# Performance work log

Measured on AMD Instinct MI355X. Metric: run time of the kernel, lower is better.

The kernel has to match this reference:

```python
import jax, jax.numpy as jnp
import numpy as np

N_NODES = 100000
N_EDGES = 1000000
IN_DIM, HID_DIM, OUT_DIM = 64, 64, 128


def gcn_conv(x, W, b, src, dst, deg_inv_sqrt, n_nodes):
    # PyG GCNConv: x' = D^{-1/2} (A + I) D^{-1/2} (x W) + b
    xw = x @ W  # [N, out]
    norm = deg_inv_sqrt[src] * deg_inv_sqrt[dst]  # [E'] (edges incl. self-loops)
    msgs = xw[src] * norm[:, None]  # gather + scale, [E', out]
    out = jax.ops.segment_sum(msgs, dst, num_segments=n_nodes)
    return out + b


def setup_inputs() -> dict:
    key = jax.random.key(0)
    ks = jax.random.split(key, 8)
    x = jax.random.normal(ks[0], (N_NODES, IN_DIM), dtype=jnp.float32)
    edge_index = jax.random.randint(ks[1], (2, N_EDGES), 0, N_NODES, dtype=jnp.int64 if jax.config.read('jax_enable_x64') else jnp.int32)
    # Glorot-ish init for weights, zeros for biases (matches GCNConv defaults)
    def glorot(k, fan_in, fan_out):
        s = jnp.sqrt(6.0 / (fan_in + fan_out))
        return jax.random.uniform(k, (fan_in, fan_out), jnp.float32, -s, s)
    return {
        "x": x,
        "W1": glorot(ks[2], IN_DIM, HID_DIM), "b1": jnp.zeros((HID_DIM,), jnp.float32),
        "W2": glorot(ks[3], HID_DIM, HID_DIM), "b2": jnp.zeros((HID_DIM,), jnp.float32),
        "W3": glorot(ks[4], HID_DIM, OUT_DIM), "b3": jnp.zeros((OUT_DIM,), jnp.float32),
        "edge_index": edge_index,
    }


def reference(x, W1, b1, W2, b2, W3, b3, edge_index):
    n = x.shape[0]
    loop = jnp.arange(n, dtype=edge_index.dtype)
    src = jnp.concatenate([edge_index[0], loop])  # add self-loops
    dst = jnp.concatenate([edge_index[1], loop])
    deg = jax.ops.segment_sum(jnp.ones_like(dst, dtype=x.dtype), dst, num_segments=n)
    deg_inv_sqrt = jnp.where(deg > 0, jax.lax.rsqrt(deg), 0.0)
    # Dropout(p=0.5) is identity in eval mode
    h = jax.nn.relu(gcn_conv(x, W1, b1, src, dst, deg_inv_sqrt, n))
    h = jax.nn.relu(gcn_conv(h, W2, b2, src, dst, deg_inv_sqrt, n))
    return gcn_conv(h, W3, b3, src, dst, deg_inv_sqrt, n)
```

## Files before the change

### kernel.cpp

```cpp
#include <hip/hip_runtime.h>
#include <hip/hip_fp16.h>


#define NBMAX 512
#define EPB   4096


__global__ __launch_bounds__(256) void bin_hist(const int* __restrict__ dst,
                                                int* __restrict__ hist, int E, int NB) {
  __shared__ int cnt[NBMAX];
  for (int i = threadIdx.x; i < NB; i += 256) cnt[i] = 0;
  __syncthreads();
  int base = blockIdx.x * EPB;
  for (int it = 0; it < EPB; it += 256) {
    int e = base + it + threadIdx.x;
    if (e < E) atomicAdd(&cnt[dst[e] >> 8], 1);
  }
  __syncthreads();
  for (int i = threadIdx.x; i < NB; i += 256) hist[(size_t)blockIdx.x * NB + i] = cnt[i];
}

__global__ __launch_bounds__(256) void bucket_prefix(int* __restrict__ hist,
                                                     int* __restrict__ bucket_tot,
                                                     int nblk, int NB) {
  __shared__ int tmp[256];
  int b = blockIdx.x;
  int t = threadIdx.x;
  int v = (t < nblk) ? hist[(size_t)t * NB + b] : 0;
  tmp[t] = v;
  __syncthreads();
  for (int off = 1; off < 256; off <<= 1) {
    int a = (t >= off) ? tmp[t - off] : 0;
    __syncthreads();
    tmp[t] += a;
    __syncthreads();
  }
  if (t < nblk) hist[(size_t)t * NB + b] = tmp[t] - v;
  if (t == 255) bucket_tot[b] = tmp[255];
}

__global__ __launch_bounds__(512) void bucket_scan(const int* __restrict__ bucket_tot,
                                                   int* __restrict__ bucket_off, int NB, int E) {
  __shared__ int tmp[NBMAX];
  int t = threadIdx.x;
  int v = (t < NB) ? bucket_tot[t] : 0;
  tmp[t] = v;
  __syncthreads();
  for (int off = 1; off < 512; off <<= 1) {
    int a = (t >= off) ? tmp[t - off] : 0;
    __syncthreads();
    tmp[t] += a;
    __syncthreads();
  }
  if (t < NB) bucket_off[t] = tmp[t] - v;
  if (t == 0) bucket_off[NB] = E;
}

__global__ __launch_bounds__(256) void bin_scatter(const int* __restrict__ src,
                                                   const int* __restrict__ dst,
                                                   const int* __restrict__ chunk_excl,
                                                   const int* __restrict__ bucket_off,
                                                   int* __restrict__ pairs, int E, int NB) {
  __shared__ int cur[NBMAX];
  for (int i = threadIdx.x; i < NB; i += 256)
    cur[i] = bucket_off[i] + chunk_excl[(size_t)blockIdx.x * NB + i];
  __syncthreads();
  int base = blockIdx.x * EPB;
  for (int it = 0; it < EPB; it += 256) {
    int e = base + it + threadIdx.x;
    if (e < E) {
      int d = dst[e];
      int pos = atomicAdd(&cur[d >> 8], 1);
      pairs[pos] = src[e] | ((d & 255) << 17);
    }
  }
}

__device__ __forceinline__ unsigned int packh(float a, float b) {
  unsigned int lo = (unsigned int)__half_as_ushort(__float2half_rn(a));
  unsigned int hi = (unsigned int)__half_as_ushort(__float2half_rn(b));
  return lo | (hi << 16);
}

__device__ __forceinline__ void unpack_add(float& x0, float& x1, unsigned int u) {
  x0 += __half2float(__ushort_as_half((unsigned short)(u & 0xffffu)));
  x1 += __half2float(__ushort_as_half((unsigned short)(u >> 16)));
}

__global__ __launch_bounds__(256) void bucket_fill(const int* __restrict__ pairs,
                                                   const int* __restrict__ bucket_off,
                                                   int* __restrict__ row_ptr,
                                                   int* __restrict__ csr_src,
                                                   float* __restrict__ dis,
                                                   const float* __restrict__ x,
                                                   unsigned short* __restrict__ xs,
                                                   int n, int NB) {
  __shared__ int cnt[256];
  __shared__ int tmp[256];
  __shared__ int cur[256];
  __shared__ float sdis[256];
  int b = blockIdx.x;
  int t = threadIdx.x;
  int node_base = b << 8;
  int ebeg = bucket_off[b];
  int eend = bucket_off[b + 1];
  cnt[t] = 0;
  __syncthreads();
  for (int e = ebeg + t; e < eend; e += 256) {
    atomicAdd(&cnt[(pairs[e] >> 17) & 255], 1);
  }
  __syncthreads();
  int v = cnt[t];
  tmp[t] = v;
  __syncthreads();
  for (int off = 1; off < 256; off <<= 1) {
    int a = (t >= off) ? tmp[t - off] : 0;
    __syncthreads();
    tmp[t] += a;
    __syncthreads();
  }
  int excl = tmp[t] - v;
  int node = node_base + t;
  float s = rsqrtf((float)v + 1.0f);
  sdis[t] = s;
  if (node < n) {
    row_ptr[node] = ebeg + excl;
    dis[node] = s;
  }
  cur[t] = ebeg + excl;
  if (b == NB - 1 && t == 0) row_ptr[n] = eend;
  __syncthreads();
  for (int e = ebeg + t; e < eend; e += 256) {
    int p = pairs[e];
    int pos = atomicAdd(&cur[(p >> 17) & 255], 1);
    csr_src[pos] = p & 0x1FFFF;
  }
  int rows = n - node_base;
  if (rows > 256) rows = 256;
  for (int i = t; i < rows * 8; i += 256) {
    int r = i >> 3;
    float sc = sdis[r];
    const float4* p = (const float4*)(x + ((size_t)(node_base + r) * 64) + (i & 7) * 8);
    float4 f0 = p[0];
    float4 f1 = p[1];
    uint4 u;
    u.x = packh(f0.x * sc, f0.y * sc);
    u.y = packh(f0.z * sc, f0.w * sc);
    u.z = packh(f1.x * sc, f1.y * sc);
    u.w = packh(f1.z * sc, f1.w * sc);
    *(uint4*)(xs + (size_t)(node_base + r) * 64 + (i & 7) * 8) = u;
  }
}


__global__ __launch_bounds__(256) void gather64q(const int* __restrict__ row_ptr,
                                                 const int* __restrict__ csr_src,
                                                 const unsigned short* __restrict__ in,
                                                 const float* __restrict__ dis,
                                                 float* __restrict__ agg, int n) {
  int node = blockIdx.x * 16 + (threadIdx.x >> 4);
  int l15 = threadIdx.x & 15;
  int gbase = threadIdx.x & 48;
  if (node >= n) return;

  int beg = row_ptr[node];
  int end = row_ptr[node + 1];

  float a0 = 0.f, a1 = 0.f, a2 = 0.f, a3 = 0.f;

  {
    uint2 q = *(const uint2*)(in + (size_t)node * 64 + l15 * 4);
    unpack_add(a0, a1, q.x); unpack_add(a2, a3, q.y);
  }

  int k = beg;
  for (; k + 16 <= end; k += 16) {
    int idx = csr_src[k + l15];
#pragma unroll
    for (int rr = 0; rr < 16; rr += 2) {
      int s0 = __shfl(idx, gbase + rr);
      int s1 = __shfl(idx, gbase + rr + 1);
      uint2 q0 = *(const uint2*)(in + (size_t)s0 * 64 + l15 * 4);
      uint2 q1 = *(const uint2*)(in + (size_t)s1 * 64 + l15 * 4);
      unpack_add(a0, a1, q0.x); unpack_add(a2, a3, q0.y);
      unpack_add(a0, a1, q1.x); unpack_add(a2, a3, q1.y);
    }
  }
  int cnt = end - k;
  if (cnt > 0) {
    int ii = k + l15;
    int last = end - 1;
    ii = (ii < end) ? ii : last;
    int idx = csr_src[ii];
#pragma unroll
    for (int rr = 0; rr < 16; rr += 2) {
      int s0 = __shfl(idx, gbase + rr);
      int s1 = __shfl(idx, gbase + rr + 1);
      uint2 q0 = *(const uint2*)(in + (size_t)s0 * 64 + l15 * 4);
      uint2 q1 = *(const uint2*)(in + (size_t)s1 * 64 + l15 * 4);
      q0.x = (rr < cnt) ? q0.x : 0u;
      q0.y = (rr < cnt) ? q0.y : 0u;
      q1.x = (rr + 1 < cnt) ? q1.x : 0u;
      q1.y = (rr + 1 < cnt) ? q1.y : 0u;
      unpack_add(a0, a1, q0.x); unpack_add(a2, a3, q0.y);
      unpack_add(a0, a1, q1.x); unpack_add(a2, a3, q1.y);
    }
  }

  float sc = dis[node];
  *(float4*)&agg[(size_t)node * 64 + l15 * 4] =
      make_float4(a0 * sc, a1 * sc, a2 * sc, a3 * sc);
}


__device__ __forceinline__ void fma4(float4& a, float s, const float4 w) {
  a.x = fmaf(s, w.x, a.x);
  a.y = fmaf(s, w.y, a.y);
  a.z = fmaf(s, w.z, a.z);
  a.w = fmaf(s, w.w, a.w);
}

template <bool RELU, bool SCALE, bool OUTH>
__global__ __launch_bounds__(256, 4) void gemm64(const float* __restrict__ X,
                                                 const float* __restrict__ W,
                                                 const float* __restrict__ B,
                                                 const float* __restrict__ dis,
                                                 float* __restrict__ yF,
                                                 unsigned short* __restrict__ yH,
                                                 int n, int ldw) {
  __shared__ float Ws[64 * 64];
  int tid = threadIdx.x;
  int rb = blockIdx.x * 64;
  int cb = blockIdx.y * 64;

  for (int i = tid; i < 1024; i += 256) {
    int k = i >> 4, cq = (i & 15) << 2;
    *(float4*)&Ws[k * 64 + cq] = *(const float4*)&W[(size_t)k * ldw + cb + cq];
  }
  __syncthreads();

  int r0 = (tid >> 4) << 2;
  int c0 = (tid & 15) << 2;
  int gr0 = rb + r0;

  const float* xp0 = X + (size_t)min(gr0 + 0, n - 1) * 64;
  const float* xp1 = X + (size_t)min(gr0 + 1, n - 1) * 64;
  const float* xp2 = X + (size_t)min(gr0 + 2, n - 1) * 64;
  const float* xp3 = X + (size_t)min(gr0 + 3, n - 1) * 64;

  float4 a0 = make_float4(0.f, 0.f, 0.f, 0.f);
  float4 a1 = a0, a2 = a0, a3 = a0;

#pragma unroll 2
  for (int kc = 0; kc < 64; kc += 4) {
    float4 x0 = *(const float4*)(xp0 + kc);
    float4 x1 = *(const float4*)(xp1 + kc);
    float4 x2 = *(const float4*)(xp2 + kc);
    float4 x3 = *(const float4*)(xp3 + kc);
    float4 w0 = *(const float4*)&Ws[(kc + 0) * 64 + c0];
    float4 w1 = *(const float4*)&Ws[(kc + 1) * 64 + c0];
    float4 w2 = *(const float4*)&Ws[(kc + 2) * 64 + c0];
    float4 w3 = *(const float4*)&Ws[(kc + 3) * 64 + c0];
    fma4(a0, x0.x, w0); fma4(a0, x0.y, w1); fma4(a0, x0.z, w2); fma4(a0, x0.w, w3);
    fma4(a1, x1.x, w0); fma4(a1, x1.y, w1); fma4(a1, x1.z, w2); fma4(a1, x1.w, w3);
    fma4(a2, x2.x, w0); fma4(a2, x2.y, w1); fma4(a2, x2.z, w2); fma4(a2, x2.w, w3);
    fma4(a3, x3.x, w0); fma4(a3, x3.y, w1); fma4(a3, x3.z, w2); fma4(a3, x3.w, w3);
  }

  float4 bb = *(const float4*)&B[cb + c0];
#pragma unroll
  for (int ri = 0; ri < 4; ++ri) {
    int gr = gr0 + ri;
    if (gr >= n) break;
    float4 v = (ri == 0) ? a0 : (ri == 1) ? a1 : (ri == 2) ? a2 : a3;
    v.x += bb.x; v.y += bb.y; v.z += bb.z; v.w += bb.w;
    if (RELU) {
      v.x = fmaxf(v.x, 0.f); v.y = fmaxf(v.y, 0.f);
      v.z = fmaxf(v.z, 0.f); v.w = fmaxf(v.w, 0.f);
    }
    if (SCALE) {
      float s = dis[gr];
      v.x *= s; v.y *= s; v.z *= s; v.w *= s;
    }
    if (OUTH) {
      uint2 u;
      u.x = packh(v.x, v.y);
      u.y = packh(v.z, v.w);
      *(uint2*)(yH + (size_t)gr * ldw + cb + c0) = u;
    } else {
      *(float4*)&yF[(size_t)gr * ldw + cb + c0] = v;
    }
  }
}


extern "C" void kernel_launch(void* const* d_in, const int* in_sizes, int n_in,
                              void* d_out, int out_size, void* d_ws, size_t ws_size,
                              hipStream_t stream) {
  const float* x  = (const float*)d_in[0];
  const float* W1 = (const float*)d_in[1];
  const float* b1 = (const float*)d_in[2];
  const float* W2 = (const float*)d_in[3];
  const float* b2 = (const float*)d_in[4];
  const float* W3 = (const float*)d_in[5];
  const float* b3 = (const float*)d_in[6];
  const int*   ei = (const int*)d_in[7];

  const int n = in_sizes[0] / 64;
  const int E = in_sizes[7] / 2;
  const int* src = ei;
  const int* dst = ei + E;

  const int NB    = (n + 255) >> 8;
  const int nblkA = (E + EPB - 1) / EPB;

  float* dis = (float*)d_ws;
  unsigned short* bufIn = (unsigned short*)(dis + n);
  float* agg = (float*)(bufIn + (size_t)n * 64);
  int* row_ptr = (int*)(agg + (size_t)n * 64);
  int* csr_src = row_ptr + (n + 2);
  int* pairs   = csr_src + E;
  int* hist       = pairs + E;
  int* bucket_tot = hist + (size_t)nblkA * NB;
  int* bucket_off = bucket_tot + NB;
  float* out = (float*)d_out;

  dim3 blk(256);
  int gW = (n + 15) / 16;
  int gT = (n + 63) / 64;

  bin_hist<<<nblkA, blk, 0, stream>>>(dst, hist, E, NB);
  bucket_prefix<<<NB, blk, 0, stream>>>(hist, bucket_tot, nblkA, NB);
  bucket_scan<<<1, 512, 0, stream>>>(bucket_tot, bucket_off, NB, E);
  bin_scatter<<<nblkA, blk, 0, stream>>>(src, dst, hist, bucket_off, pairs, E, NB);
  bucket_fill<<<NB, blk, 0, stream>>>(pairs, bucket_off, row_ptr, csr_src, dis, x, bufIn, n, NB);

  gather64q<<<gW, blk, 0, stream>>>(row_ptr, csr_src, bufIn, dis, agg, n);
  gemm64<true, true, true><<<dim3(gT, 1), blk, 0, stream>>>(agg, W1, b1, dis, nullptr, bufIn, n, 64);

  gather64q<<<gW, blk, 0, stream>>>(row_ptr, csr_src, bufIn, dis, agg, n);
  gemm64<true, true, true><<<dim3(gT, 1), blk, 0, stream>>>(agg, W2, b2, dis, nullptr, bufIn, n, 64);

  gather64q<<<gW, blk, 0, stream>>>(row_ptr, csr_src, bufIn, dis, agg, n);
  gemm64<false, false, false><<<dim3(gT, 2), blk, 0, stream>>>(agg, W3, b3, dis, out, nullptr, n, 128);
}
```

Measured before the change: 278.3 us.

## Fuse neighbor gather and dense transform into one per-layer kernel

Merges the aggregation kernel and the following GEMM into a single kernel per layer. Each block aggregates 64 nodes into shared memory, then multiplies that tile by W held in shared memory. This removes the fp32 intermediate aggregate buffer round-trip and three kernel launches. Because a layer now reads and writes the same half-precision feature array, ping-pong buffers are used. The cost is heavier shared memory use (up to about 50KB for the last layer) and a larger gather per block, which may lower occupancy and latency hiding for the random gathers.

```diff
diff --git a/kernel.cpp b/kernel.cpp
--- a/kernel.cpp
+++ b/kernel.cpp
@@ -153,89 +153,73 @@
 }
 
 
-__global__ __launch_bounds__(256) void gather64q(const int* __restrict__ row_ptr,
-                                                 const int* __restrict__ csr_src,
-                                                 const unsigned short* __restrict__ in,
-                                                 const float* __restrict__ dis,
-                                                 float* __restrict__ agg, int n) {
-  int node = blockIdx.x * 16 + (threadIdx.x >> 4);
-  int l15 = threadIdx.x & 15;
-  int gbase = threadIdx.x & 48;
-  if (node >= n) return;
-
-  int beg = row_ptr[node];
-  int end = row_ptr[node + 1];
-
-  float a0 = 0.f, a1 = 0.f, a2 = 0.f, a3 = 0.f;
-
-  {
-    uint2 q = *(const uint2*)(in + (size_t)node * 64 + l15 * 4);
-    unpack_add(a0, a1, q.x); unpack_add(a2, a3, q.y);
-  }
-
-  int k = beg;
-  for (; k + 16 <= end; k += 16) {
-    int idx = csr_src[k + l15];
-#pragma unroll
-    for (int rr = 0; rr < 16; rr += 2) {
-      int s0 = __shfl(idx, gbase + rr);
-      int s1 = __shfl(idx, gbase + rr + 1);
-      uint2 q0 = *(const uint2*)(in + (size_t)s0 * 64 + l15 * 4);
-      uint2 q1 = *(const uint2*)(in + (size_t)s1 * 64 + l15 * 4);
-      unpack_add(a0, a1, q0.x); unpack_add(a2, a3, q0.y);
-      unpack_add(a0, a1, q1.x); unpack_add(a2, a3, q1.y);
-    }
-  }
-  int cnt = end - k;
-  if (cnt > 0) {
-    int ii = k + l15;
-    int last = end - 1;
-    ii = (ii < end) ? ii : last;
-    int idx = csr_src[ii];
-#pragma unroll
-    for (int rr = 0; rr < 16; rr += 2) {
-      int s0 = __shfl(idx, gbase + rr);
-      int s1 = __shfl(idx, gbase + rr + 1);
-      uint2 q0 = *(const uint2*)(in + (size_t)s0 * 64 + l15 * 4);
-      uint2 q1 = *(const uint2*)(in + (size_t)s1 * 64 + l15 * 4);
-      q0.x = (rr < cnt) ? q0.x : 0u;
-      q0.y = (rr < cnt) ? q0.y : 0u;
-      q1.x = (rr + 1 < cnt) ? q1.x : 0u;
-      q1.y = (rr + 1 < cnt) ? q1.y : 0u;
-      unpack_add(a0, a1, q0.x); unpack_add(a2, a3, q0.y);
-      unpack_add(a0, a1, q1.x); unpack_add(a2, a3, q1.y);
-    }
-  }
-
-  float sc = dis[node];
-  *(float4*)&agg[(size_t)node * 64 + l15 * 4] =
-      make_float4(a0 * sc, a1 * sc, a2 * sc, a3 * sc);
-}
-
-
-__device__ __forceinline__ void fma4(float4& a, float s, const float4 w) {
-  a.x = fmaf(s, w.x, a.x);
-  a.y = fmaf(s, w.y, a.y);
-  a.z = fmaf(s, w.z, a.z);
-  a.w = fmaf(s, w.w, a.w);
-}
-
-template <bool RELU, bool SCALE, bool OUTH>
-__global__ __launch_bounds__(256, 4) void gemm64(const float* __restrict__ X,
-                                                 const float* __restrict__ W,
-                                                 const float* __restrict__ B,
-                                                 const float* __restrict__ dis,
-                                                 float* __restrict__ yF,
-                                                 unsigned short* __restrict__ yH,
-                                                 int n, int ldw) {
-  __shared__ float Ws[64 * 64];
+template <bool RELU, bool SCALE, bool OUTH, int NCB>
+__global__ __launch_bounds__(256, 4) void gcn_layer(
+    const int* __restrict__ row_ptr, const int* __restrict__ csr_src,
+    const unsigned short* __restrict__ in, const float* __restrict__ dis,
+    const float* __restrict__ W, const float* __restrict__ Bv,
+    float* __restrict__ yF, unsigned short* __restrict__ yH, int n) {
+  __shared__ float Xs[64 * 68];
+  __shared__ float Ws[64 * 64 * NCB];
   int tid = threadIdx.x;
   int rb = blockIdx.x * 64;
-  int cb = blockIdx.y * 64;
-
-  for (int i = tid; i < 1024; i += 256) {
-    int k = i >> 4, cq = (i & 15) << 2;
-    *(float4*)&Ws[k * 64 + cq] = *(const float4*)&W[(size_t)k * ldw + cb + cq];
+
+  for (int i = tid; i < 64 * 16 * NCB; i += 256) {
+    int k = i / (16 * NCB);
+    int cq = (i % (16 * NCB)) << 2;
+    *(float4*)&Ws[k * (64 * NCB) + cq] = *(const float4*)&W[(size_t)k * (64 * NCB) + cq];
+  }
+
+  int l15 = tid & 15;
+  int gbase = tid & 48;
+  int grp = tid >> 4;
+  for (int it = 0; it < 4; ++it) {
+    int r = it * 16 + grp;
+    int cl = min(rb + r, n - 1);
+    int beg = row_ptr[cl];
+    int end = row_ptr[cl + 1];
+
+    float a0 = 0.f, a1 = 0.f, a2 = 0.f, a3 = 0.f;
+    {
+      uint2 q = *(const uint2*)(in + (size_t)cl * 64 + l15 * 4);
+      unpack_add(a0, a1, q.x); unpack_add(a2, a3, q.y);
+    }
+    int k = beg;
+    for (; k + 16 <= end; k += 16) {
+      int idx = csr_src[k + l15];
+#pragma unroll
+      for (int rr = 0; rr < 16; rr += 2) {
+        int s0 = __shfl(idx, gbase + rr);
+        int s1 = __shfl(idx, gbase + rr + 1);
+        uint2 q0 = *(const uint2*)(in + (size_t)s0 * 64 + l15 * 4);
+        uint2 q1 = *(const uint2*)(in + (size_t)s1 * 64 + l15 * 4);
+        unpack_add(a0, a1, q0.x); unpack_add(a2, a3, q0.y);
+        unpack_add(a0, a1, q1.x); unpack_add(a2, a3, q1.y);
+      }
+    }
+    int cnt = end - k;
+    if (cnt > 0) {
+      int ii = k + l15;
+      int last = end - 1;
+      ii = (ii < end) ? ii : last;
+      int idx = csr_src[ii];
+#pragma unroll
+      for (int rr = 0; rr < 16; rr += 2) {
+        int s0 = __shfl(idx, gbase + rr);
+        int s1 = __shfl(idx, gbase + rr + 1);
+        uint2 q0 = *(const uint2*)(in + (size_t)s0 * 64 + l15 * 4);
+        uint2 q1 = *(const uint2*)(in + (size_t)s1 * 64 + l15 * 4);
+        q0.x = (rr < cnt) ? q0.x : 0u;
+        q0.y = (rr < cnt) ? q0.y : 0u;
+        q1.x = (rr + 1 < cnt) ? q1.x : 0u;
+        q1.y = (rr + 1 < cnt) ? q1.y : 0u;
+        unpack_add(a0, a1, q0.x); unpack_add(a2, a3, q0.y);
+        unpack_add(a0, a1, q1.x); unpack_add(a2, a3, q1.y);
+      }
+    }
+    float sc = dis[cl];
+    *(float4*)&Xs[r * 68 + l15 * 4] =
+        make_float4(a0 * sc, a1 * sc, a2 * sc, a3 * sc);
   }
   __syncthreads();
 
@@ -243,52 +227,79 @@
   int c0 = (tid & 15) << 2;
   int gr0 = rb + r0;
 
-  const float* xp0 = X + (size_t)min(gr0 + 0, n - 1) * 64;
-  const float* xp1 = X + (size_t)min(gr0 + 1, n - 1) * 64;
-  const float* xp2 = X + (size_t)min(gr0 + 2, n - 1) * 64;
-  const float* xp3 = X + (size_t)min(gr0 + 3, n - 1) * 64;
-
-  float4 a0 = make_float4(0.f, 0.f, 0.f, 0.f);
-  float4 a1 = a0, a2 = a0, a3 = a0;
+#pragma unroll
+  for (int cb = 0; cb < NCB; ++cb) {
+    float4 a0 = make_float4(0.f, 0.f, 0.f, 0.f);
+    float4 a1 = a0, a2 = a0, a3 = a0;
 
 #pragma unroll 2
-  for (int kc = 0; kc < 64; kc += 4) {
-    float4 x0 = *(const float4*)(xp0 + kc);
-    float4 x1 = *(const float4*)(xp1 + kc);
-    float4 x2 = *(const float4*)(xp2 + kc);
-    float4 x3 = *(const float4*)(xp3 + kc);
-    float4 w0 = *(const float4*)&Ws[(kc + 0) * 64 + c0];
-    float4 w1 = *(const float4*)&Ws[(kc + 1) * 64 + c0];
-    float4 w2 = *(const float4*)&Ws[(kc + 2) * 64 + c0];
-    float4 w3 = *(const float4*)&Ws[(kc + 3) * 64 + c0];
-    fma4(a0, x0.x, w0); fma4(a0, x0.y, w1); fma4(a0, x0.z, w2); fma4(a0, x0.w, w3);
-    fma4(a1, x1.x, w0); fma4(a1, x1.y, w1); fma4(a1, x1.z, w2); fma4(a1, x1.w, w3);
-    fma4(a2, x2.x, w0); fma4(a2, x2.y, w1); fma4(a2, x2.z, w2); fma4(a2, x2.w, w3);
-    fma4(a3, x3.x, w0); fma4(a3, x3.y, w1); fma4(a3, x3.z, w2); fma4(a3, x3.w, w3);
-  }
-
-  float4 bb = *(const float4*)&B[cb + c0];
+    for (int kc = 0; kc < 64; kc += 4) {
+      float4 x0 = *(const float4*)&Xs[(r0 + 0) * 68 + kc];
+      float4 x1 = *(const float4*)&Xs[(r0 + 1) * 68 + kc];
+      float4 x2 = *(const float4*)&Xs[(r0 + 2) * 68 + kc];
+      float4 x3 = *(const float4*)&Xs[(r0 + 3) * 68 + kc];
+      const float* wp = &Ws[(size_t)kc * (64 * NCB) + cb * 64 + c0];
+      float4 w0 = *(const float4*)(wp + 0 * (64 * NCB));
+      float4 w1 = *(const float4*)(wp + 1 * (64 * NCB));
+      float4 w2 = *(const float4*)(wp + 2 * (64 * NCB));
+      float4 w3 = *(const float4*)(wp + 3 * (64 * NCB));
+      a0.x = fmaf(x0.x, w0.x, a0.x); a0.y = fmaf(x0.x, w0.y, a0.y);
+      a0.z = fmaf(x0.x, w0.z, a0.z); a0.w = fmaf(x0.x, w0.w, a0.w);
+      a0.x = fmaf(x0.y, w1.x, a0.x); a0.y = fmaf(x0.y, w1.y, a0.y);
+      a0.z = fmaf(x0.y, w1.z, a0.z); a0.w = fmaf(x0.y, w1.w, a0.w);
+      a0.x = fmaf(x0.z, w2.x, a0.x); a0.y = fmaf(x0.z, w2.y, a0.y);
+      a0.z = fmaf(x0.z, w2.z, a0.z); a0.w = fmaf(x0.z, w2.w, a0.w);
+      a0.x = fmaf(x0.w, w3.x, a0.x); a0.y = fmaf(x0.w, w3.y, a0.y);
+      a0.z = fmaf(x0.w, w3.z, a0.z); a0.w = fmaf(x0.w, w3.w, a0.w);
+      a1.x = fmaf(x1.x, w0.x, a1.x); a1.y = fmaf(x1.x, w0.y, a1.y);
+      a1.z = fmaf(x1.x, w0.z, a1.z); a1.w = fmaf(x1.x, w0.w, a1.w);
+      a1.x = fmaf(x1.y, w1.x, a1.x); a1.y = fmaf(x1.y, w1.y, a1.y);
+      a1.z = fmaf(x1.y, w1.z, a1.z); a1.w = fmaf(x1.y, w1.w, a1.w);
+      a1.x = fmaf(x1.z, w2.x, a1.x); a1.y = fmaf(x1.z, w2.y, a1.y);
+      a1.z = fmaf(x1.z, w2.z, a1.z); a1.w = fmaf(x1.z, w2.w, a1.w);
+      a1.x = fmaf(x1.w, w3.x, a1.x); a1.y = fmaf(x1.w, w3.y, a1.y);
+      a1.z = fmaf(x1.w, w3.z, a1.z); a1.w = fmaf(x1.w, w3.w, a1.w);
+      a2.x = fmaf(x2.x, w0.x, a2.x); a2.y = fmaf(x2.x, w0.y, a2.y);
+      a2.z = fmaf(x2.x, w0.z, a2.z); a2.w = fmaf(x2.x, w0.w, a2.w);
+      a2.x = fmaf(x2.y, w1.x, a2.x); a2.y = fmaf(x2.y, w1.y, a2.y);
+      a2.z = fmaf(x2.y, w1.z, a2.z); a2.w = fmaf(x2.y, w1.w, a2.w);
+      a2.x = fmaf(x2.z, w2.x, a2.x); a2.y = fmaf(x2.z, w2.y, a2.y);
+      a2.z = fmaf(x2.z, w2.z, a2.z); a2.w = fmaf(x2.z, w2.w, a2.w);
+      a2.x = fmaf(x2.w, w3.x, a2.x); a2.y = fmaf(x2.w, w3.y, a2.y);
+      a2.z = fmaf(x2.w, w3.z, a2.z); a2.w = fmaf(x2.w, w3.w, a2.w);
+      a3.x = fmaf(x3.x, w0.x, a3.x); a3.y = fmaf(x3.x, w0.y, a3.y);
+      a3.z = fmaf(x3.x, w0.z, a3.z); a3.w = fmaf(x3.x, w0.w, a3.w);
+      a3.x = fmaf(x3.y, w1.x, a3.x); a3.y = fmaf(x3.y, w1.y, a3.y);
+      a3.z = fmaf(x3.y, w1.z, a3.z); a3.w = fmaf(x3.y, w1.w, a3.w);
+      a3.x = fmaf(x3.z, w2.x, a3.x); a3.y = fmaf(x3.z, w2.y, a3.y);
+      a3.z = fmaf(x3.z, w2.z, a3.z); a3.w = fmaf(x3.z, w2.w, a3.w);
+      a3.x = fmaf(x3.w, w3.x, a3.x); a3.y = fmaf(x3.w, w3.y, a3.y);
+      a3.z = fmaf(x3.w, w3.z, a3.z); a3.w = fmaf(x3.w, w3.w, a3.w);
+    }
+
+    float4 bb = *(const float4*)&Bv[cb * 64 + c0];
 #pragma unroll
-  for (int ri = 0; ri < 4; ++ri) {
-    int gr = gr0 + ri;
-    if (gr >= n) break;
-    float4 v = (ri == 0) ? a0 : (ri == 1) ? a1 : (ri == 2) ? a2 : a3;
-    v.x += bb.x; v.y += bb.y; v.z += bb.z; v.w += bb.w;
-    if (RELU) {
-      v.x = fmaxf(v.x, 0.f); v.y = fmaxf(v.y, 0.f);
-      v.z = fmaxf(v.z, 0.f); v.w = fmaxf(v.w, 0.f);
-    }
-    if (SCALE) {
-      float s = dis[gr];
-      v.x *= s; v.y *= s; v.z *= s; v.w *= s;
-    }
-    if (OUTH) {
-      uint2 u;
-      u.x = packh(v.x, v.y);
-      u.y = packh(v.z, v.w);
-      *(uint2*)(yH + (size_t)gr * ldw + cb + c0) = u;
-    } else {
-      *(float4*)&yF[(size_t)gr * ldw + cb + c0] = v;
+    for (int ri = 0; ri < 4; ++ri) {
+      int gr = gr0 + ri;
+      if (gr >= n) break;
+      float4 v = (ri == 0) ? a0 : (ri == 1) ? a1 : (ri == 2) ? a2 : a3;
+      v.x += bb.x; v.y += bb.y; v.z += bb.z; v.w += bb.w;
+      if (RELU) {
+        v.x = fmaxf(v.x, 0.f); v.y = fmaxf(v.y, 0.f);
+        v.z = fmaxf(v.z, 0.f); v.w = fmaxf(v.w, 0.f);
+      }
+      if (SCALE) {
+        float s = dis[gr];
+        v.x *= s; v.y *= s; v.z *= s; v.w *= s;
+      }
+      if (OUTH) {
+        uint2 u;
+        u.x = packh(v.x, v.y);
+        u.y = packh(v.z, v.w);
+        *(uint2*)(yH + (size_t)gr * 64 + c0) = u;
+      } else {
+        *(float4*)&yF[(size_t)gr * (64 * NCB) + cb * 64 + c0] = v;
+      }
     }
   }
 }
@@ -315,9 +326,9 @@
   const int nblkA = (E + EPB - 1) / EPB;
 
   float* dis = (float*)d_ws;
-  unsigned short* bufIn = (unsigned short*)(dis + n);
-  float* agg = (float*)(bufIn + (size_t)n * 64);
-  int* row_ptr = (int*)(agg + (size_t)n * 64);
+  unsigned short* bufA = (unsigned short*)(dis + n);
+  unsigned short* bufB = bufA + (size_t)n * 64;
+  int* row_ptr = (int*)(bufB + (size_t)n * 64);
   int* csr_src = row_ptr + (n + 2);
   int* pairs   = csr_src + E;
   int* hist       = pairs + E;
@@ -326,21 +337,20 @@
   float* out = (float*)d_out;
 
   dim3 blk(256);
-  int gW = (n + 15) / 16;
-  int gT = (n + 63) / 64;
+  int gL = (n + 63) / 64;
 
   bin_hist<<<nblkA, blk, 0, stream>>>(dst, hist, E, NB);
   bucket_prefix<<<NB, blk, 0, stream>>>(hist, bucket_tot, nblkA, NB);
   bucket_scan<<<1, 512, 0, stream>>>(bucket_tot, bucket_off, NB, E);
   bin_scatter<<<nblkA, blk, 0, stream>>>(src, dst, hist, bucket_off, pairs, E, NB);
-  bucket_fill<<<NB, blk, 0, stream>>>(pairs, bucket_off, row_ptr, csr_src, dis, x, bufIn, n, NB);
-
-  gather64q<<<gW, blk, 0, stream>>>(row_ptr, csr_src, bufIn, dis, agg, n);
-  gemm64<true, true, true><<<dim3(gT, 1), blk, 0, stream>>>(agg, W1, b1, dis, nullptr, bufIn, n, 64);
-
-  gather64q<<<gW, blk, 0, stream>>>(row_ptr, csr_src, bufIn, dis, agg, n);
-  gemm64<true, true, true><<<dim3(gT, 1), blk, 0, stream>>>(agg, W2, b2, dis, nullptr, bufIn, n, 64);
-
-  gather64q<<<gW, blk, 0, stream>>>(row_ptr, csr_src, bufIn, dis, agg, n);
-  gemm64<false, false, false><<<dim3(gT, 2), blk, 0, stream>>>(agg, W3, b3, dis, out, nullptr, n, 128);
-}
+  bucket_fill<<<NB, blk, 0, stream>>>(pairs, bucket_off, row_ptr, csr_src, dis, x, bufA, n, NB);
+
+  gcn_layer<true, true, true, 1><<<gL, blk, 0, stream>>>(
+      row_ptr, csr_src, bufA, dis, W1, b1, nullptr, bufB, n);
+
+  gcn_layer<true, true, true, 1><<<gL, blk, 0, stream>>>(
+      row_ptr, csr_src, bufB, dis, W2, b2, nullptr, bufA, n);
+
+  gcn_layer<false, false, false, 2><<<gL, blk, 0, stream>>>(
+      row_ptr, csr_src, bufA, dis, W3, b3, out, nullptr, n);
+}
```

Measured after the change: 253.4 us. -9.0%, faster.
